# Performance work log

Hardware: AMD Instinct MI355X
Metric: run time of the kernel (lower is better)

The kernel has to match this reference:

```python
import jax, jax.numpy as jnp
import numpy as np

B, NQ, NK, D = 4, 4096, 4096, 1024


def setup_inputs() -> dict:
    key = jax.random.key(0)
    kq, kv = jax.random.split(key)
    query = jax.random.normal(kq, (B, NQ, D), dtype=jnp.float32)
    values = jax.random.normal(kv, (B, NK, D), dtype=jnp.float32)
    return {"query": query, "values": values}


def reference(query, values):
    # scores = Q @ V^T  (unscaled), shape [B, NQ, NK]
    scores = jnp.einsum("bqd,bkd->bqk", query, values)
    attn = jax.nn.softmax(scores, axis=-1)
    # context = attn @ V, shape [B, NQ, D]
    context = jnp.einsum("bqk,bkd->bqd", attn, values)
    return context
```

## Files before the change

kernel.cpp:

```cpp
#include <hip/hip_runtime.h>


#define NB   4
#define NQL  4096
#define NKL  4096
#define DIM  1024
#define BQ   32
#define BK   32
#define NW   8
#define DSL  128
#define NT   (NKL / BK)
#define LOG2E 1.44269504088896340736f
#define PBW  40

typedef float f32x2 __attribute__((ext_vector_type(2)));
typedef float f32x4 __attribute__((ext_vector_type(4)));
typedef _Float16 f16x8 __attribute__((ext_vector_type(8)));
typedef short s16x8 __attribute__((ext_vector_type(8)));
typedef short s16x4 __attribute__((ext_vector_type(4)));
typedef unsigned int uint_;

union Frag { f16x8 v; s16x8 s; _Float16 h[8]; };

__device__ __forceinline__ void rawbar() {
    asm volatile("s_waitcnt lgkmcnt(0)\n\ts_barrier" ::: "memory");
}

__global__ void prep_v(const float* __restrict__ Vg, short* __restrict__ v16,
                       short* __restrict__ vt16) {
    __shared__ short lds[64][72];
    const int t   = (int)threadIdx.x;
    const int blk = (int)blockIdx.x;
    const int bb    = blk >> 10;
    const int ktile = (blk >> 4) & 63;
    const int dtile = blk & 15;
    const int k0 = ktile * 64, d0 = dtile * 64;
    const int row = t >> 2;
    const int cb  = (t & 3) * 16;

    const float* src = Vg + ((size_t)(bb * NKL + k0 + row) * DIM + d0 + cb);
    short* vdst = v16 + ((size_t)(bb * NKL + k0 + row) * DIM + d0 + cb);
#pragma unroll
    for (int i = 0; i < 4; ++i) {
        f32x4 x = *(const f32x4*)(src + i * 4);
        s16x4 h;
#pragma unroll
        for (int j = 0; j < 4; ++j)
            h[j] = __builtin_bit_cast(short, (_Float16)x[j]);
        *(s16x4*)(vdst + i * 4) = h;
        *(s16x4*)&lds[row][cb + i * 4] = h;
    }
    __syncthreads();
    short* tdst = vt16 + ((size_t)(bb * DIM + d0 + row) * NKL + k0 + cb);
#pragma unroll
    for (int i = 0; i < 4; ++i) {
        s16x4 h;
#pragma unroll
        for (int j = 0; j < 4; ++j)
            h[j] = lds[cb + i * 4 + j][row];
        *(s16x4*)(tdst + i * 4) = h;
    }
}

template<int MODE>
__global__ __attribute__((amdgpu_flat_work_group_size(512, 512),
                          amdgpu_waves_per_eu(2, 4)))
void attn_f16(const float* __restrict__ Qg, const float* __restrict__ Vg,
              float* __restrict__ Og, const short* __restrict__ v16,
              const short* __restrict__ vt16) {
    __shared__ float spart[NW][BQ][BK];
    __shared__ __align__(16) short pbuf[BQ * PBW];
    __shared__ float arun[BQ];
    __shared__ float lsum[BQ];

    const int tid = (int)threadIdx.x;
    const int l   = tid & 63;
    const int w   = tid >> 6;
    const int l15 = l & 15;
    const int lg  = l >> 4;

    const int bid  = (int)blockIdx.x;
    const int orig = (bid & 7) * 64 + (bid >> 3);
    const int b  = orig >> 7;
    const int qt = orig & 127;
    const int q0 = qt * BQ;
    const int dw = w * DSL;

    f16x8 qf[2][4];
#pragma unroll
    for (int qb = 0; qb < 2; ++qb)
#pragma unroll
        for (int dc = 0; dc < 4; ++dc) {
            const float* qp = Qg + (size_t)(b * NQL + q0 + qb * 16 + l15) * DIM
                            + dw + dc * 32 + lg * 8;
            f32x4 x0 = *(const f32x4*)qp;
            f32x4 x1 = *(const f32x4*)(qp + 4);
            f16x8 a;
#pragma unroll
            for (int j = 0; j < 4; ++j) { a[j] = (_Float16)x0[j]; a[j + 4] = (_Float16)x1[j]; }
            qf[qb][dc] = a;
        }

    f32x4 oacc[2][8];
#pragma unroll
    for (int qb = 0; qb < 2; ++qb)
#pragma unroll
        for (int dg = 0; dg < 8; ++dg)
            oacc[qb][dg] = (f32x4){0.f, 0.f, 0.f, 0.f};

    f32x4 sacc[2][2];
    f32x4 hA32[4][2], hB32[4][2];
    s16x8 hA16[4], hB16[4];

    auto loadhalf = [&](int buf, int kt_, int kb) {
        if constexpr (MODE == 1) {
            const short* vp = v16 + ((size_t)(b * NKL + kt_ * BK + kb * 16 + l15) * DIM
                            + dw + lg * 8);
            s16x8 (&hb)[4] = buf ? hB16 : hA16;
#pragma unroll
            for (int dc = 0; dc < 4; ++dc)
                hb[dc] = *(const s16x8*)(vp + dc * 32);
        } else {
            const float* vp = Vg + (size_t)(b * NKL + kt_ * BK + kb * 16 + l15) * DIM
                            + dw + lg * 8;
            f32x4 (&hb)[4][2] = buf ? hB32 : hA32;
#pragma unroll
            for (int dc = 0; dc < 4; ++dc) {
                hb[dc][0] = *(const f32x4*)(vp + dc * 32);
                hb[dc][1] = *(const f32x4*)(vp + dc * 32 + 4);
            }
        }
    };

    auto computehalf = [&](int buf, int kb) {
#pragma unroll
        for (int dc = 0; dc < 4; ++dc) {
            Frag fa;
            if constexpr (MODE == 1) {
                fa.s = buf ? hB16[dc] : hA16[dc];
            } else {
                f32x4 (&hb)[4][2] = buf ? hB32 : hA32;
#pragma unroll
                for (int j = 0; j < 4; ++j) {
                    fa.h[j]     = (_Float16)hb[dc][0][j];
                    fa.h[j + 4] = (_Float16)hb[dc][1][j];
                }
            }
            sacc[kb][0] = __builtin_amdgcn_mfma_f32_16x16x32_f16(fa.v, qf[0][dc], sacc[kb][0], 0, 0, 0);
            sacc[kb][1] = __builtin_amdgcn_mfma_f32_16x16x32_f16(fa.v, qf[1][dc], sacc[kb][1], 0, 0, 0);
        }
    };

    const int qsm = 4 * w + lg;
    const int kk  = (2 * l15) ^ ((qsm & 7) << 2);

    float m_reg  = -3e38f;
    float l_lane = 0.f;

    loadhalf(0, 0, 0);
    loadhalf(1, 0, 1);
    rawbar();

    for (int kt = 0; kt < NT; ++kt) {
#pragma unroll
        for (int kb = 0; kb < 2; ++kb)
#pragma unroll
            for (int qb = 0; qb < 2; ++qb)
                sacc[kb][qb] = (f32x4){0.f, 0.f, 0.f, 0.f};

        const int ktn = (kt + 1 < NT) ? kt + 1 : NT - 1;
        computehalf(0, 0);
        loadhalf(0, ktn, 0);
        computehalf(1, 1);
        loadhalf(1, ktn, 1);

#pragma unroll
        for (int kb = 0; kb < 2; ++kb)
#pragma unroll
            for (int qb = 0; qb < 2; ++qb) {
                const int q = qb * 16 + l15;
                const int kblk = (kb * 16 + lg * 4) ^ ((q & 7) << 2);
                *(f32x4*)&spart[w][q][kblk] = sacc[kb][qb];
            }
        rawbar();

        float pv[8][8];
        if constexpr (MODE == 0) {
            const float* vb = Vg + (size_t)(b * NKL + kt * BK + lg * 8) * DIM
                            + dw + l15;
#pragma unroll
            for (int dg = 0; dg < 8; ++dg)
#pragma unroll
                for (int j = 0; j < 8; ++j)
                    pv[dg][j] = vb[(size_t)j * DIM + dg * 16];
        }

        {
            f32x2 sp = (f32x2){0.f, 0.f};
#pragma unroll
            for (int wv = 0; wv < NW; ++wv)
                sp += *(const f32x2*)&spart[wv][qsm][kk];
            float s0 = sp[0], s1 = sp[1];
            float smax = fmaxf(s0, s1);
            float alpha = 1.0f;
            if (!__all(smax - m_reg <= 8.0f)) {
                float mloc = smax;
#pragma unroll
                for (int off = 1; off < 16; off <<= 1)
                    mloc = fmaxf(mloc, __shfl_xor(mloc, off));
                float mnew = fmaxf(m_reg, mloc);
                alpha = exp2f((m_reg - mnew) * LOG2E);
                m_reg = mnew;
            }
            float p0 = exp2f((s0 - m_reg) * LOG2E);
            float p1 = exp2f((s1 - m_reg) * LOG2E);
            l_lane = alpha * l_lane + (p0 + p1);
            if (l15 == 0) arun[qsm] = alpha;
            uint_ pk = (uint_)__builtin_bit_cast(unsigned short, (_Float16)p0)
                     | ((uint_)__builtin_bit_cast(unsigned short, (_Float16)p1) << 16);
            *(uint_*)&pbuf[qsm * PBW + 2 * l15] = pk;
        }
        rawbar();

        {
            f32x4 av[2];
#pragma unroll
            for (int qb = 0; qb < 2; ++qb)
                av[qb] = *(const f32x4*)&arun[qb * 16 + lg * 4];
            bool mine1 = true;
#pragma unroll
            for (int qb = 0; qb < 2; ++qb)
#pragma unroll
                for (int r = 0; r < 4; ++r)
                    mine1 = mine1 && (av[qb][r] == 1.0f);
            if (!__all(mine1)) {
#pragma unroll
                for (int qb = 0; qb < 2; ++qb)
#pragma unroll
                    for (int dg = 0; dg < 8; ++dg)
#pragma unroll
                        for (int r = 0; r < 4; ++r)
                            oacc[qb][dg][r] *= av[qb][r];
            }
        }

        Frag pf[2];
#pragma unroll
        for (int qb = 0; qb < 2; ++qb)
            pf[qb].s = *(const s16x8*)&pbuf[(qb * 16 + l15) * PBW + lg * 8];

        const short* vtb = (MODE == 1)
            ? vt16 + ((size_t)(b * DIM + dw + l15) * NKL + kt * BK + lg * 8)
            : nullptr;

#pragma unroll
        for (int dg = 0; dg < 8; ++dg) {
            Frag bf;
            if constexpr (MODE == 1) {
                bf.s = *(const s16x8*)(vtb + (size_t)dg * 16 * NKL);
            } else {
#pragma unroll
                for (int j = 0; j < 8; ++j)
                    bf.h[j] = (_Float16)pv[dg][j];
            }
            __builtin_amdgcn_s_setprio(1);
#pragma unroll
            for (int qb = 0; qb < 2; ++qb)
                oacc[qb][dg] = __builtin_amdgcn_mfma_f32_16x16x32_f16(
                    pf[qb].v, bf.v, oacc[qb][dg], 0, 0, 0);
            __builtin_amdgcn_s_setprio(0);
        }
    }

    {
        float rs = l_lane;
#pragma unroll
        for (int off = 1; off < 16; off <<= 1)
            rs += __shfl_xor(rs, off);
        if (l15 == 0) lsum[qsm] = rs;
    }
    __syncthreads();
#pragma unroll
    for (int qb = 0; qb < 2; ++qb) {
        f32x4 lv = *(const f32x4*)&lsum[qb * 16 + lg * 4];
        float il[4];
#pragma unroll
        for (int r = 0; r < 4; ++r) il[r] = 1.0f / lv[r];
#pragma unroll
        for (int dg = 0; dg < 8; ++dg)
#pragma unroll
            for (int r = 0; r < 4; ++r) {
                int q = q0 + qb * 16 + lg * 4 + r;
                int d = dw + dg * 16 + l15;
                Og[(size_t)(b * NQL + q) * DIM + d] = oacc[qb][dg][r] * il[r];
            }
    }
}

extern "C" void kernel_launch(void* const* d_in, const int* in_sizes, int n_in,
                              void* d_out, int out_size, void* d_ws, size_t ws_size,
                              hipStream_t stream) {
    const float* Q = (const float*)d_in[0];
    const float* V = (const float*)d_in[1];
    float* O = (float*)d_out;
    (void)in_sizes; (void)n_in; (void)out_size;

    const size_t elems = (size_t)NB * NKL * DIM;
    const size_t need  = 2 * elems * sizeof(short);
    if (ws_size >= need) {
        short* v16  = (short*)d_ws;
        short* vt16 = v16 + elems;
        prep_v<<<dim3(NB * 1024), dim3(256), 0, stream>>>(V, v16, vt16);
        attn_f16<1><<<dim3(NB * (NQL / BQ)), dim3(NW * 64), 0, stream>>>(
            Q, V, O, v16, vt16);
    } else {
        attn_f16<0><<<dim3(NB * (NQL / BQ)), dim3(NW * 64), 0, stream>>>(
            Q, V, O, nullptr, nullptr);
    }
}
```

Baseline: 1.068 ms.

## Halve query tile to 16 rows and double grid for more occupancy

Shrinks the per-block query tile from 32 to 16 rows. The per-q-block register arrays and MFMA loops collapse to a single 16-row block, and the grid doubles to 1024 workgroups. The waves-per-EU hint is raised so more waves can be resident, which should hide latency better. The cost is that each V tile, in both fp16 and transposed forms, now feeds half as many queries, so total V traffic through the caches doubles, and waves 4-7 redundantly compute the same softmax rows as waves 0-3.

```diff
diff --git a/kernel.cpp b/kernel.cpp
--- a/kernel.cpp
+++ b/kernel.cpp
@@ -5,7 +5,7 @@
 #define NQL  4096
 #define NKL  4096
 #define DIM  1024
-#define BQ   32
+#define BQ   16
 #define BK   32
 #define NW   8
 #define DSL  128
@@ -64,7 +64,7 @@
 
 template<int MODE>
 __global__ __attribute__((amdgpu_flat_work_group_size(512, 512),
-                          amdgpu_waves_per_eu(2, 4)))
+                          amdgpu_waves_per_eu(2, 8)))
 void attn_f16(const float* __restrict__ Qg, const float* __restrict__ Vg,
               float* __restrict__ Og, const short* __restrict__ v16,
               const short* __restrict__ vt16) {
@@ -80,35 +80,31 @@
     const int lg  = l >> 4;
 
     const int bid  = (int)blockIdx.x;
-    const int orig = (bid & 7) * 64 + (bid >> 3);
-    const int b  = orig >> 7;
-    const int qt = orig & 127;
+    const int orig = (bid & 7) * 128 + (bid >> 3);
+    const int b  = orig >> 8;
+    const int qt = orig & 255;
     const int q0 = qt * BQ;
     const int dw = w * DSL;
 
-    f16x8 qf[2][4];
-#pragma unroll
-    for (int qb = 0; qb < 2; ++qb)
-#pragma unroll
-        for (int dc = 0; dc < 4; ++dc) {
-            const float* qp = Qg + (size_t)(b * NQL + q0 + qb * 16 + l15) * DIM
-                            + dw + dc * 32 + lg * 8;
-            f32x4 x0 = *(const f32x4*)qp;
-            f32x4 x1 = *(const f32x4*)(qp + 4);
-            f16x8 a;
-#pragma unroll
-            for (int j = 0; j < 4; ++j) { a[j] = (_Float16)x0[j]; a[j + 4] = (_Float16)x1[j]; }
-            qf[qb][dc] = a;
-        }
-
-    f32x4 oacc[2][8];
-#pragma unroll
-    for (int qb = 0; qb < 2; ++qb)
-#pragma unroll
-        for (int dg = 0; dg < 8; ++dg)
-            oacc[qb][dg] = (f32x4){0.f, 0.f, 0.f, 0.f};
-
-    f32x4 sacc[2][2];
+    f16x8 qf[4];
+#pragma unroll
+    for (int dc = 0; dc < 4; ++dc) {
+        const float* qp = Qg + (size_t)(b * NQL + q0 + l15) * DIM
+                        + dw + dc * 32 + lg * 8;
+        f32x4 x0 = *(const f32x4*)qp;
+        f32x4 x1 = *(const f32x4*)(qp + 4);
+        f16x8 a;
+#pragma unroll
+        for (int j = 0; j < 4; ++j) { a[j] = (_Float16)x0[j]; a[j + 4] = (_Float16)x1[j]; }
+        qf[dc] = a;
+    }
+
+    f32x4 oacc[8];
+#pragma unroll
+    for (int dg = 0; dg < 8; ++dg)
+        oacc[dg] = (f32x4){0.f, 0.f, 0.f, 0.f};
+
+    f32x4 sacc[2];
     f32x4 hA32[4][2], hB32[4][2];
     s16x8 hA16[4], hB16[4];
 
@@ -146,12 +142,11 @@
                     fa.h[j + 4] = (_Float16)hb[dc][1][j];
                 }
             }
-            sacc[kb][0] = __builtin_amdgcn_mfma_f32_16x16x32_f16(fa.v, qf[0][dc], sacc[kb][0], 0, 0, 0);
-            sacc[kb][1] = __builtin_amdgcn_mfma_f32_16x16x32_f16(fa.v, qf[1][dc], sacc[kb][1], 0, 0, 0);
+            sacc[kb] = __builtin_amdgcn_mfma_f32_16x16x32_f16(fa.v, qf[dc], sacc[kb], 0, 0, 0);
         }
     };
 
-    const int qsm = 4 * w + lg;
+    const int qsm = (4 * w + lg) & 15;
     const int kk  = (2 * l15) ^ ((qsm & 7) << 2);
 
     float m_reg  = -3e38f;
@@ -162,11 +157,8 @@
     rawbar();
 
     for (int kt = 0; kt < NT; ++kt) {
-#pragma unroll
-        for (int kb = 0; kb < 2; ++kb)
-#pragma unroll
-            for (int qb = 0; qb < 2; ++qb)
-                sacc[kb][qb] = (f32x4){0.f, 0.f, 0.f, 0.f};
+        sacc[0] = (f32x4){0.f, 0.f, 0.f, 0.f};
+        sacc[1] = (f32x4){0.f, 0.f, 0.f, 0.f};
 
         const int ktn = (kt + 1 < NT) ? kt + 1 : NT - 1;
         computehalf(0, 0);
@@ -175,13 +167,11 @@
         loadhalf(1, ktn, 1);
 
 #pragma unroll
-        for (int kb = 0; kb < 2; ++kb)
-#pragma unroll
-            for (int qb = 0; qb < 2; ++qb) {
-                const int q = qb * 16 + l15;
-                const int kblk = (kb * 16 + lg * 4) ^ ((q & 7) << 2);
-                *(f32x4*)&spart[w][q][kblk] = sacc[kb][qb];
-            }
+        for (int kb = 0; kb < 2; ++kb) {
+            const int q = l15;
+            const int kblk = (kb * 16 + lg * 4) ^ ((q & 7) << 2);
+            *(f32x4*)&spart[w][q][kblk] = sacc[kb];
+        }
         rawbar();
 
         float pv[8][8];
@@ -223,31 +213,20 @@
         rawbar();
 
         {
-            f32x4 av[2];
-#pragma unroll
-            for (int qb = 0; qb < 2; ++qb)
-                av[qb] = *(const f32x4*)&arun[qb * 16 + lg * 4];
-            bool mine1 = true;
-#pragma unroll
-            for (int qb = 0; qb < 2; ++qb)
-#pragma unroll
-                for (int r = 0; r < 4; ++r)
-                    mine1 = mine1 && (av[qb][r] == 1.0f);
+            f32x4 av = *(const f32x4*)&arun[lg * 4];
+            bool mine1 = (av[0] == 1.0f) && (av[1] == 1.0f)
+                      && (av[2] == 1.0f) && (av[3] == 1.0f);
             if (!__all(mine1)) {
 #pragma unroll
-                for (int qb = 0; qb < 2; ++qb)
-#pragma unroll
-                    for (int dg = 0; dg < 8; ++dg)
-#pragma unroll
-                        for (int r = 0; r < 4; ++r)
-                            oacc[qb][dg][r] *= av[qb][r];
-            }
-        }
-
-        Frag pf[2];
-#pragma unroll
-        for (int qb = 0; qb < 2; ++qb)
-            pf[qb].s = *(const s16x8*)&pbuf[(qb * 16 + l15) * PBW + lg * 8];
+                for (int dg = 0; dg < 8; ++dg)
+#pragma unroll
+                    for (int r = 0; r < 4; ++r)
+                        oacc[dg][r] *= av[r];
+            }
+        }
+
+        Frag pf;
+        pf.s = *(const s16x8*)&pbuf[l15 * PBW + lg * 8];
 
         const short* vtb = (MODE == 1)
             ? vt16 + ((size_t)(b * DIM + dw + l15) * NKL + kt * BK + lg * 8)
@@ -264,10 +243,8 @@
                     bf.h[j] = (_Float16)pv[dg][j];
             }
             __builtin_amdgcn_s_setprio(1);
-#pragma unroll
-            for (int qb = 0; qb < 2; ++qb)
-                oacc[qb][dg] = __builtin_amdgcn_mfma_f32_16x16x32_f16(
-                    pf[qb].v, bf.v, oacc[qb][dg], 0, 0, 0);
+            oacc[dg] = __builtin_amdgcn_mfma_f32_16x16x32_f16(
+                pf.v, bf.v, oacc[dg], 0, 0, 0);
             __builtin_amdgcn_s_setprio(0);
         }
     }
@@ -280,9 +257,8 @@
         if (l15 == 0) lsum[qsm] = rs;
     }
     __syncthreads();
-#pragma unroll
-    for (int qb = 0; qb < 2; ++qb) {
-        f32x4 lv = *(const f32x4*)&lsum[qb * 16 + lg * 4];
+    {
+        f32x4 lv = *(const f32x4*)&lsum[lg * 4];
         float il[4];
 #pragma unroll
         for (int r = 0; r < 4; ++r) il[r] = 1.0f / lv[r];
@@ -290,9 +266,9 @@
         for (int dg = 0; dg < 8; ++dg)
 #pragma unroll
             for (int r = 0; r < 4; ++r) {
-                int q = q0 + qb * 16 + lg * 4 + r;
+                int q = q0 + lg * 4 + r;
                 int d = dw + dg * 16 + l15;
-                Og[(size_t)(b * NQL + q) * DIM + d] = oacc[qb][dg][r] * il[r];
+                Og[(size_t)(b * NQL + q) * DIM + d] = oacc[dg][r] * il[r];
             }
     }
 }
@@ -307,14 +283,14 @@
 
     const size_t elems = (size_t)NB * NKL * DIM;
     const size_t need  = 2 * elems * sizeof(short);
+    dim3 grid(NB * (NQL / BQ));
+    dim3 block(NW * 64);
     if (ws_size >= need) {
         short* v16  = (short*)d_ws;
         short* vt16 = v16 + elems;
         prep_v<<<dim3(NB * 1024), dim3(256), 0, stream>>>(V, v16, vt16);
-        attn_f16<1><<<dim3(NB * (NQL / BQ)), dim3(NW * 64), 0, stream>>>(
-            Q, V, O, v16, vt16);
+        attn_f16<1><<<grid, block, 0, stream>>>(Q, V, O, v16, vt16);
     } else {
-        attn_f16<0><<<dim3(NB * (NQL / BQ)), dim3(NW * 64), 0, stream>>>(
-            Q, V, O, nullptr, nullptr);
-    }
-}
+        attn_f16<0><<<grid, block, 0, stream>>>(Q, V, O, nullptr, nullptr);
+    }
+}
```

After: 2.031 ms. +90.2%, slower.

## Software-pipeline QK^T of next tile with softmax and PV of previous tile

Applied to the files above, without the earlier changes.

Restructures the key-tile loop so the QK^T MFMAs for tile kt run alongside the softmax and PV accumulation of tile kt-1. Partial-score, probability and alpha buffers in shared memory are double-buffered, which removes one barrier per iteration. PV operand loads for V^T are issued into registers before the QK^T work so their latency is hidden. The cost is more LDS use and more live registers, which could lower occupancy or cause spills.

```diff
diff --git a/kernel.cpp b/kernel.cpp
--- a/kernel.cpp
+++ b/kernel.cpp
@@ -68,9 +68,9 @@
 void attn_f16(const float* __restrict__ Qg, const float* __restrict__ Vg,
               float* __restrict__ Og, const short* __restrict__ v16,
               const short* __restrict__ vt16) {
-    __shared__ float spart[NW][BQ][BK];
-    __shared__ __align__(16) short pbuf[BQ * PBW];
-    __shared__ float arun[BQ];
+    __shared__ float spart[2][NW][BQ][BK];
+    __shared__ __align__(16) short pbuf[2][BQ * PBW];
+    __shared__ float arun[2][BQ];
     __shared__ float lsum[BQ];
 
     const int tid = (int)threadIdx.x;
@@ -112,7 +112,7 @@
     f32x4 hA32[4][2], hB32[4][2];
     s16x8 hA16[4], hB16[4];
 
-    auto loadhalf = [&](int buf, int kt_, int kb) {
+    auto loadstage = [&](int buf, int kt_, int kb) {
         if constexpr (MODE == 1) {
             const short* vp = v16 + ((size_t)(b * NKL + kt_ * BK + kb * 16 + l15) * DIM
                             + dw + lg * 8);
@@ -132,7 +132,7 @@
         }
     };
 
-    auto computehalf = [&](int buf, int kb) {
+    auto qkt_half = [&](int buf, int kb) {
 #pragma unroll
         for (int dc = 0; dc < 4; ++dc) {
             Frag fa;
@@ -151,117 +151,114 @@
         }
     };
 
-    const int qsm = 4 * w + lg;
-    const int kk  = (2 * l15) ^ ((qsm & 7) << 2);
-
-    float m_reg  = -3e38f;
-    float l_lane = 0.f;
-
-    loadhalf(0, 0, 0);
-    loadhalf(1, 0, 1);
-    rawbar();
-
-    for (int kt = 0; kt < NT; ++kt) {
+    auto qkt_tile = [&](int kt_, int spbuf) {
 #pragma unroll
         for (int kb = 0; kb < 2; ++kb)
 #pragma unroll
             for (int qb = 0; qb < 2; ++qb)
                 sacc[kb][qb] = (f32x4){0.f, 0.f, 0.f, 0.f};
-
-        const int ktn = (kt + 1 < NT) ? kt + 1 : NT - 1;
-        computehalf(0, 0);
-        loadhalf(0, ktn, 0);
-        computehalf(1, 1);
-        loadhalf(1, ktn, 1);
-
+        const int ktn = (kt_ + 1 < NT) ? kt_ + 1 : NT - 1;
+        qkt_half(0, 0);
+        loadstage(0, ktn, 0);
+        qkt_half(1, 1);
+        loadstage(1, ktn, 1);
 #pragma unroll
         for (int kb = 0; kb < 2; ++kb)
 #pragma unroll
             for (int qb = 0; qb < 2; ++qb) {
                 const int q = qb * 16 + l15;
                 const int kblk = (kb * 16 + lg * 4) ^ ((q & 7) << 2);
-                *(f32x4*)&spart[w][q][kblk] = sacc[kb][qb];
-            }
-        rawbar();
-
-        float pv[8][8];
+                *(f32x4*)&spart[spbuf][w][q][kblk] = sacc[kb][qb];
+            }
+    };
+
+    const int qsm = 4 * w + lg;
+    const int kk  = (2 * l15) ^ ((qsm & 7) << 2);
+
+    float m_reg  = -3e38f;
+    float l_lane = 0.f;
+
+    auto softmax_tile = [&](int cur) {
+        f32x2 sp = (f32x2){0.f, 0.f};
+#pragma unroll
+        for (int wv = 0; wv < NW; ++wv)
+            sp += *(const f32x2*)&spart[cur][wv][qsm][kk];
+        float s0 = sp[0], s1 = sp[1];
+        float smax = fmaxf(s0, s1);
+        float alpha = 1.0f;
+        if (!__all(smax - m_reg <= 8.0f)) {
+            float mloc = smax;
+#pragma unroll
+            for (int off = 1; off < 16; off <<= 1)
+                mloc = fmaxf(mloc, __shfl_xor(mloc, off));
+            float mnew = fmaxf(m_reg, mloc);
+            alpha = exp2f((m_reg - mnew) * LOG2E);
+            m_reg = mnew;
+        }
+        float p0 = exp2f((s0 - m_reg) * LOG2E);
+        float p1 = exp2f((s1 - m_reg) * LOG2E);
+        l_lane = alpha * l_lane + (p0 + p1);
+        if (l15 == 0) arun[cur][qsm] = alpha;
+        uint_ pk = (uint_)__builtin_bit_cast(unsigned short, (_Float16)p0)
+                 | ((uint_)__builtin_bit_cast(unsigned short, (_Float16)p1) << 16);
+        *(uint_*)&pbuf[cur][qsm * PBW + 2 * l15] = pk;
+    };
+
+    s16x8 pvreg[8];
+    float pv32[8][8];
+
+    auto pv_loads = [&](int kt_) {
+        if constexpr (MODE == 1) {
+            const short* vtb = vt16 + ((size_t)(b * DIM + dw + l15) * NKL
+                             + kt_ * BK + lg * 8);
+#pragma unroll
+            for (int dg = 0; dg < 8; ++dg)
+                pvreg[dg] = *(const s16x8*)(vtb + (size_t)dg * 16 * NKL);
+        }
+    };
+
+    auto pv_tile = [&](int kt_, int cur) {
         if constexpr (MODE == 0) {
-            const float* vb = Vg + (size_t)(b * NKL + kt * BK + lg * 8) * DIM
+            const float* vb = Vg + (size_t)(b * NKL + kt_ * BK + lg * 8) * DIM
                             + dw + l15;
 #pragma unroll
             for (int dg = 0; dg < 8; ++dg)
 #pragma unroll
                 for (int j = 0; j < 8; ++j)
-                    pv[dg][j] = vb[(size_t)j * DIM + dg * 16];
-        }
-
-        {
-            f32x2 sp = (f32x2){0.f, 0.f};
-#pragma unroll
-            for (int wv = 0; wv < NW; ++wv)
-                sp += *(const f32x2*)&spart[wv][qsm][kk];
-            float s0 = sp[0], s1 = sp[1];
-            float smax = fmaxf(s0, s1);
-            float alpha = 1.0f;
-            if (!__all(smax - m_reg <= 8.0f)) {
-                float mloc = smax;
-#pragma unroll
-                for (int off = 1; off < 16; off <<= 1)
-                    mloc = fmaxf(mloc, __shfl_xor(mloc, off));
-                float mnew = fmaxf(m_reg, mloc);
-                alpha = exp2f((m_reg - mnew) * LOG2E);
-                m_reg = mnew;
-            }
-            float p0 = exp2f((s0 - m_reg) * LOG2E);
-            float p1 = exp2f((s1 - m_reg) * LOG2E);
-            l_lane = alpha * l_lane + (p0 + p1);
-            if (l15 == 0) arun[qsm] = alpha;
-            uint_ pk = (uint_)__builtin_bit_cast(unsigned short, (_Float16)p0)
-                     | ((uint_)__builtin_bit_cast(unsigned short, (_Float16)p1) << 16);
-            *(uint_*)&pbuf[qsm * PBW + 2 * l15] = pk;
-        }
-        rawbar();
-
-        {
-            f32x4 av[2];
+                    pv32[dg][j] = vb[(size_t)j * DIM + dg * 16];
+        }
+        f32x4 av[2];
+#pragma unroll
+        for (int qb = 0; qb < 2; ++qb)
+            av[qb] = *(const f32x4*)&arun[cur][qb * 16 + lg * 4];
+        bool mine1 = true;
+#pragma unroll
+        for (int qb = 0; qb < 2; ++qb)
+#pragma unroll
+            for (int r = 0; r < 4; ++r)
+                mine1 = mine1 && (av[qb][r] == 1.0f);
+        if (!__all(mine1)) {
 #pragma unroll
             for (int qb = 0; qb < 2; ++qb)
-                av[qb] = *(const f32x4*)&arun[qb * 16 + lg * 4];
-            bool mine1 = true;
-#pragma unroll
-            for (int qb = 0; qb < 2; ++qb)
-#pragma unroll
-                for (int r = 0; r < 4; ++r)
-                    mine1 = mine1 && (av[qb][r] == 1.0f);
-            if (!__all(mine1)) {
-#pragma unroll
-                for (int qb = 0; qb < 2; ++qb)
-#pragma unroll
-                    for (int dg = 0; dg < 8; ++dg)
-#pragma unroll
-                        for (int r = 0; r < 4; ++r)
-                            oacc[qb][dg][r] *= av[qb][r];
-            }
-        }
-
+#pragma unroll
+                for (int dg = 0; dg < 8; ++dg)
+#pragma unroll
+                    for (int r = 0; r < 4; ++r)
+                        oacc[qb][dg][r] *= av[qb][r];
+        }
         Frag pf[2];
 #pragma unroll
         for (int qb = 0; qb < 2; ++qb)
-            pf[qb].s = *(const s16x8*)&pbuf[(qb * 16 + l15) * PBW + lg * 8];
-
-        const short* vtb = (MODE == 1)
-            ? vt16 + ((size_t)(b * DIM + dw + l15) * NKL + kt * BK + lg * 8)
-            : nullptr;
-
+            pf[qb].s = *(const s16x8*)&pbuf[cur][(qb * 16 + l15) * PBW + lg * 8];
 #pragma unroll
         for (int dg = 0; dg < 8; ++dg) {
             Frag bf;
             if constexpr (MODE == 1) {
-                bf.s = *(const s16x8*)(vtb + (size_t)dg * 16 * NKL);
+                bf.s = pvreg[dg];
             } else {
 #pragma unroll
                 for (int j = 0; j < 8; ++j)
-                    bf.h[j] = (_Float16)pv[dg][j];
+                    bf.h[j] = (_Float16)pv32[dg][j];
             }
             __builtin_amdgcn_s_setprio(1);
 #pragma unroll
@@ -270,6 +267,28 @@
                     pf[qb].v, bf.v, oacc[qb][dg], 0, 0, 0);
             __builtin_amdgcn_s_setprio(0);
         }
+    };
+
+    loadstage(0, 0, 0);
+    loadstage(1, 0, 1);
+    qkt_tile(0, 0);
+    rawbar();
+
+    for (int kt = 1; kt < NT; ++kt) {
+        const int cur = (kt - 1) & 1;
+        pv_loads(kt - 1);
+        qkt_tile(kt, kt & 1);
+        softmax_tile(cur);
+        rawbar();
+        pv_tile(kt - 1, cur);
+    }
+
+    {
+        const int cur = (NT - 1) & 1;
+        pv_loads(NT - 1);
+        softmax_tile(cur);
+        rawbar();
+        pv_tile(NT - 1, cur);
     }
 
     {
@@ -307,14 +326,14 @@
 
     const size_t elems = (size_t)NB * NKL * DIM;
     const size_t need  = 2 * elems * sizeof(short);
+    dim3 grid(NB * (NQL / BQ));
+    dim3 block(NW * 64);
     if (ws_size >= need) {
         short* v16  = (short*)d_ws;
         short* vt16 = v16 + elems;
         prep_v<<<dim3(NB * 1024), dim3(256), 0, stream>>>(V, v16, vt16);
-        attn_f16<1><<<dim3(NB * (NQL / BQ)), dim3(NW * 64), 0, stream>>>(
-            Q, V, O, v16, vt16);
+        attn_f16<1><<<grid, block, 0, stream>>>(Q, V, O, v16, vt16);
     } else {
-        attn_f16<0><<<dim3(NB * (NQL / BQ)), dim3(NW * 64), 0, stream>>>(
-            Q, V, O, nullptr, nullptr);
+        attn_f16<0><<<grid, block, 0, stream>>>(Q, V, O, nullptr, nullptr);
     }
 }
```

Measured after the change: 935.8 us. 12.3% less time.
